# Optimization experiments

Hardware: AMD Instinct MI355X
Metric: run time of the kernel (lower is better)

The kernel has to match this reference:

```python
import jax, jax.numpy as jnp
import numpy as np

DT = 0.01  # continuous-time step for the S4D/Vandermonde reservoir kernel


def setup_inputs() -> dict:
    key = jax.random.key(0)
    ks = jax.random.split(key, 10)
    B, H, L, N = 16, 128, 4096, 64
    u = jax.random.normal(ks[0], (B, H, L), dtype=jnp.float32)
    # stable diagonal SSM: real part of Lambda strictly negative
    lambda_re = -0.5 * jax.random.uniform(ks[1], (H, N), dtype=jnp.float32) - 0.1
    lambda_im = jax.random.normal(ks[2], (H, N), dtype=jnp.float32) * np.pi
    w_re = jax.random.normal(ks[3], (H, N), dtype=jnp.float32) / np.sqrt(N)
    w_im = jax.random.normal(ks[4], (H, N), dtype=jnp.float32) / np.sqrt(N)
    d = jax.random.normal(ks[5], (H,), dtype=jnp.float32)
    mlp_w1 = jax.random.normal(ks[6], (H, H), dtype=jnp.float32) / np.sqrt(H)
    mlp_b1 = jnp.zeros((H,), dtype=jnp.float32)
    mlp_w2 = jax.random.normal(ks[7], (H, H), dtype=jnp.float32) / np.sqrt(H)
    mlp_b2 = jnp.zeros((H,), dtype=jnp.float32)
    return {"u": u, "lambda_re": lambda_re, "lambda_im": lambda_im,
            "w_re": w_re, "w_im": w_im, "d": d,
            "mlp_w1": mlp_w1, "mlp_b1": mlp_b1,
            "mlp_w2": mlp_w2, "mlp_b2": mlp_b2}


def reference(u, lambda_re, lambda_im, w_re, w_im, d,
              mlp_w1, mlp_b1, mlp_w2, mlp_b2):
    B, H, L = u.shape
    Lam = lambda_re + 1j * lambda_im          # (H, N) diagonal state matrix
    W = w_re + 1j * w_im                      # (H, N) merged C*B readout
    ell = jnp.arange(L, dtype=jnp.float32)
    # Vandermonde kernel: K[h, l] = sum_n W[h,n] * exp(dt * Lambda[h,n] * l)
    V = jnp.exp((DT * Lam)[:, :, None] * ell[None, None, :])  # (H, N, L)
    K = jnp.einsum('hn,hnl->hl', W, V)                         # (H, L) complex
    # causal FFT convolution (pad to 2L to avoid circular wrap)
    n = 2 * L
    y = jnp.fft.ifft(jnp.fft.fft(u, n=n, axis=-1) * jnp.fft.fft(K, n=n, axis=-1)[None],
                     n=n, axis=-1)[..., :L]
    y = y + d[None, :, None] * u              # skip / feed-through term
    y = y.real                                # Real() projection
    # 1x1-conv MLP with ReLU (mlp_layers = 2)
    h1 = jax.nn.relu(jnp.einsum('oh,bhl->bol', mlp_w1, y) + mlp_b1[None, :, None])
    y2 = jax.nn.relu(jnp.einsum('oh,bhl->bol', mlp_w2, h1) + mlp_b2[None, :, None])
    return y2
```

## Files before the change

kernel.cpp:

```cpp
#include <hip/hip_runtime.h>
#include <hip/hip_bf16.h>

#define B_ 16
#define H_ 128
#define L_ 4096
#define N_ 64
#define DT_ 0.01f

typedef __bf16 bf16;
typedef __bf16 bf16x8 __attribute__((ext_vector_type(8)));
typedef __bf16 bf16x4 __attribute__((ext_vector_type(4)));
typedef float f32x4 __attribute__((ext_vector_type(4)));

__global__ void k_prep(const float* __restrict__ w1, const float* __restrict__ w2,
                       bf16* __restrict__ w1b, bf16* __restrict__ w2b) {
    int i = blockIdx.x * blockDim.x + threadIdx.x;
    if (i < H_ * H_) {
        w1b[i] = (bf16)w1[i];
        w2b[i] = (bf16)w2[i];
    }
}

__global__ __launch_bounds__(64) void k_prep2(
        const float* __restrict__ lre, const float* __restrict__ lim,
        const float* __restrict__ wre, const float* __restrict__ wim,
        bf16* __restrict__ Pbf, bf16* __restrict__ Qbf,
        float* __restrict__ tap, float* __restrict__ acre, float* __restrict__ acim) {
    __shared__ float red[64 * 65];
    const int h = blockIdx.x, n = threadIdx.x;
    const float lr = lre[h * 64 + n] * DT_, li = lim[h * 64 + n] * DT_;
    const float e = expf(lr);
    const float ar = e * cosf(li), ai = e * sinf(li);
    const float wr = wre[h * 64 + n], wi = wim[h * 64 + n];
    const float war = wr * ar - wi * ai;
    const float wai = wr * ai + wi * ar;
    float pr = 1.f, pi = 0.f;
    bf16* Ph = Pbf + (size_t)h * 128 * 64;
    bf16* Qh = Qbf + (size_t)h * 64 * 128;
    for (int dlt = 0; dlt < 64; ++dlt) {
        Ph[(size_t)n * 64 + (63 - dlt)]        = (bf16)pr;
        Ph[(size_t)(64 + n) * 64 + (63 - dlt)] = (bf16)pi;
        Qh[(size_t)dlt * 128 + 2 * n]     = (bf16)(war * pr - wai * pi);
        Qh[(size_t)dlt * 128 + 2 * n + 1] = (bf16)(-(war * pi + wai * pr));
        red[dlt * 65 + n] = wr * pr - wi * pi;
        const float npr = ar * pr - ai * pi;
        const float npi = ar * pi + ai * pr;
        pr = npr; pi = npi;
    }
    acre[h * 64 + n] = pr;
    acim[h * 64 + n] = pi;
    __syncthreads();
    float s = 0.f;
    #pragma unroll
    for (int k = 0; k < 64; ++k) s += red[n * 65 + k];
    tap[h * 64 + n] = s;
}

#define USWZ(c, k) ((c) * 64 + (((((k) >> 4) ^ ((c) & 3)) << 4) | ((k) & 15)))
#define SSWZ(c, k) ((c) * 128 + (((((k) >> 4) ^ ((c) & 7)) << 4) | ((k) & 15)))
__global__ __launch_bounds__(256) void k_ssm2(
        const float* __restrict__ u, const float* __restrict__ dv,
        const bf16* __restrict__ Pbf, const bf16* __restrict__ Qbf,
        const float* __restrict__ tap,
        const float* __restrict__ acre, const float* __restrict__ acim,
        bf16* __restrict__ ybf) {
    __shared__ bf16  Ubf[64 * 64];
    __shared__ float Ctr[128 * 65];
    __shared__ bf16  Sbf[64 * 128];
    __shared__ bf16  Tm[64 * 72];

    const int tid = threadIdx.x;
    const int bh  = blockIdx.x;
    const int h   = bh & (H_ - 1);
    const float* __restrict__ up = u + (size_t)bh * L_;

    {
        const int c = tid >> 2, j0 = (tid & 3) << 4;
        const float4* src = (const float4*)(up + c * 64 + j0);
        bf16x8 t0, t1;
        #pragma unroll
        for (int v = 0; v < 2; ++v) {
            float4 f0 = src[2 * v], f1 = src[2 * v + 1];
            bf16x8 t;
            t[0] = (bf16)f0.x; t[1] = (bf16)f0.y; t[2] = (bf16)f0.z; t[3] = (bf16)f0.w;
            t[4] = (bf16)f1.x; t[5] = (bf16)f1.y; t[6] = (bf16)f1.z; t[7] = (bf16)f1.w;
            if (v == 0) t0 = t; else t1 = t;
        }
        bf16* dst = &Ubf[USWZ(c, j0)];
        ((bf16x8*)dst)[0] = t0;
        ((bf16x8*)dst)[1] = t1;
    }
    {
        const int dlt = tid >> 2, j0 = (tid & 3) << 4;
        const float* tp = tap + h * 64;
        const float dh = dv[h];
        bf16x8 t0, t1;
        #pragma unroll
        for (int e = 0; e < 16; ++e) {
            const int j = j0 + e;
            float v = (j <= dlt) ? tp[dlt - j] : 0.f;
            if (j == dlt) v += dh;
            if (e < 8) t0[e] = (bf16)v; else t1[e - 8] = (bf16)v;
        }
        bf16* dst = &Tm[dlt * 72 + j0];
        ((bf16x8*)dst)[0] = t0;
        ((bf16x8*)dst)[1] = t1;
    }
    __syncthreads();

    const int lane = tid & 63, wv = tid >> 6;
    const int cl = lane & 15, q = lane >> 4;

    {
        f32x4 acc[2][4];
        #pragma unroll
        for (int i = 0; i < 2; ++i)
            #pragma unroll
            for (int nt = 0; nt < 4; ++nt) acc[i][nt] = (f32x4){0.f, 0.f, 0.f, 0.f};
        const bf16* Ph = Pbf + (size_t)h * 128 * 64;
        #pragma unroll
        for (int ks = 0; ks < 2; ++ks) {
            const int k0 = ks * 32 + q * 8;
            const bf16x8 a0 = *(const bf16x8*)(Ph + (size_t)(wv * 32 + cl) * 64 + k0);
            const bf16x8 a1 = *(const bf16x8*)(Ph + (size_t)(wv * 32 + 16 + cl) * 64 + k0);
            #pragma unroll
            for (int nt = 0; nt < 4; ++nt) {
                const int c = nt * 16 + cl;
                const bf16x8 bfr = *(const bf16x8*)(&Ubf[USWZ(c, k0)]);
                acc[0][nt] = __builtin_amdgcn_mfma_f32_16x16x32_bf16(a0, bfr, acc[0][nt], 0, 0, 0);
                acc[1][nt] = __builtin_amdgcn_mfma_f32_16x16x32_bf16(a1, bfr, acc[1][nt], 0, 0, 0);
            }
        }
        #pragma unroll
        for (int mt = 0; mt < 2; ++mt)
            #pragma unroll
            for (int nt = 0; nt < 4; ++nt)
                #pragma unroll
                for (int r = 0; r < 4; ++r)
                    Ctr[(wv * 32 + mt * 16 + q * 4 + r) * 65 + nt * 16 + cl] = acc[mt][nt][r];
    }
    __syncthreads();

    if (wv == 0) {
        const int n = lane;
        const float ar = acre[h * 64 + n], ai = acim[h * 64 + n];
        float sr = 0.f, si = 0.f;
        #pragma unroll 8
        for (int c = 0; c < 64; ++c) {
            bf16* sp = &Sbf[SSWZ(c, 2 * n)];
            sp[0] = (bf16)sr;
            sp[1] = (bf16)si;
            const float cr = Ctr[n * 65 + c];
            const float ci = Ctr[(64 + n) * 65 + c];
            const float nr = fmaf(ar, sr, fmaf(-ai, si, cr));
            const float ni = fmaf(ar, si, fmaf(ai, sr, ci));
            sr = nr; si = ni;
        }
    }
    __syncthreads();

    {
        f32x4 acc[4];
        #pragma unroll
        for (int nt = 0; nt < 4; ++nt) acc[nt] = (f32x4){0.f, 0.f, 0.f, 0.f};
        const bf16* Qh = Qbf + (size_t)h * 64 * 128;
        #pragma unroll
        for (int ks = 0; ks < 4; ++ks) {
            const int k0 = ks * 32 + q * 8;
            const bf16x8 a = *(const bf16x8*)(Qh + (size_t)(wv * 16 + cl) * 128 + k0);
            #pragma unroll
            for (int nt = 0; nt < 4; ++nt) {
                const int c = nt * 16 + cl;
                const bf16x8 bfr = *(const bf16x8*)(&Sbf[SSWZ(c, k0)]);
                acc[nt] = __builtin_amdgcn_mfma_f32_16x16x32_bf16(a, bfr, acc[nt], 0, 0, 0);
            }
        }
        #pragma unroll
        for (int ks = 0; ks < 2; ++ks) {
            const int k0 = ks * 32 + q * 8;
            const bf16x8 a = *(const bf16x8*)(&Tm[(wv * 16 + cl) * 72 + k0]);
            #pragma unroll
            for (int nt = 0; nt < 4; ++nt) {
                const int c = nt * 16 + cl;
                const bf16x8 bfr = *(const bf16x8*)(&Ubf[USWZ(c, k0)]);
                acc[nt] = __builtin_amdgcn_mfma_f32_16x16x32_bf16(a, bfr, acc[nt], 0, 0, 0);
            }
        }
        bf16* Yb = (bf16*)Ctr;
        #pragma unroll
        for (int nt = 0; nt < 4; ++nt) {
            const int c = nt * 16 + cl;
            bf16x4 yv;
            #pragma unroll
            for (int r = 0; r < 4; ++r) yv[r] = (bf16)acc[nt][r];
            *(bf16x4*)(&Yb[c * 68 + wv * 16 + q * 4]) = yv;
        }
    }
    __syncthreads();

    {
        const bf16* Yb = (const bf16*)Ctr;
        const int c = tid >> 2, s0 = (tid & 3) << 4;
        bf16x4 v0 = *(const bf16x4*)(&Yb[c * 68 + s0 + 0]);
        bf16x4 v1 = *(const bf16x4*)(&Yb[c * 68 + s0 + 4]);
        bf16x4 v2 = *(const bf16x4*)(&Yb[c * 68 + s0 + 8]);
        bf16x4 v3 = *(const bf16x4*)(&Yb[c * 68 + s0 + 12]);
        bf16* yp = ybf + (size_t)bh * L_ + c * 64 + s0;
        ((bf16x4*)yp)[0] = v0; ((bf16x4*)yp)[1] = v1;
        ((bf16x4*)yp)[2] = v2; ((bf16x4*)yp)[3] = v3;
    }
}

#define YSTR 136
__global__ __launch_bounds__(256) void k_mlp(
        const bf16* __restrict__ ybf,
        const bf16* __restrict__ w1b, const bf16* __restrict__ w2b,
        const float* __restrict__ b1, const float* __restrict__ b2,
        float* __restrict__ out) {
    __shared__ bf16 YT [64 * YSTR];
    __shared__ bf16 H1T[64 * YSTR];
    __shared__ float B1s[H_], B2s[H_];

    const int tid = threadIdx.x;
    const int b   = blockIdx.x >> 6;
    const int lt  = blockIdx.x & 63;
    const int l0  = lt * 64;

    if (tid < H_) { B1s[tid] = b1[tid]; B2s[tid] = b2[tid]; }

    {
        const int h  = tid >> 1;
        const int lh = (tid & 1) * 32;
        const bf16x8* src = (const bf16x8*)(ybf + ((size_t)b * H_ + h) * L_ + l0 + lh);
        #pragma unroll
        for (int v = 0; v < 4; ++v) {
            bf16x8 d = src[v];
            #pragma unroll
            for (int e = 0; e < 8; ++e) YT[(lh + v * 8 + e) * YSTR + h] = d[e];
        }
    }
    __syncthreads();

    const int lane = tid & 63;
    const int wv   = tid >> 6;
    const int m    = lane & 15;
    const int q    = lane >> 4;
    const int m0   = wv * 32;

    f32x4 acc[2][4];
    #pragma unroll
    for (int i = 0; i < 2; ++i)
        #pragma unroll
        for (int nt = 0; nt < 4; ++nt) acc[i][nt] = (f32x4){0.f, 0.f, 0.f, 0.f};

    #pragma unroll
    for (int kb = 0; kb < 4; ++kb) {
        const bf16x8 a0 = *(const bf16x8*)(w1b + (size_t)(m0 + m)      * H_ + kb * 32 + q * 8);
        const bf16x8 a1 = *(const bf16x8*)(w1b + (size_t)(m0 + 16 + m) * H_ + kb * 32 + q * 8);
        #pragma unroll
        for (int nt = 0; nt < 4; ++nt) {
            const bf16x8 bfr = *(const bf16x8*)(&YT[(nt * 16 + m) * YSTR + kb * 32 + q * 8]);
            acc[0][nt] = __builtin_amdgcn_mfma_f32_16x16x32_bf16(a0, bfr, acc[0][nt], 0, 0, 0);
            acc[1][nt] = __builtin_amdgcn_mfma_f32_16x16x32_bf16(a1, bfr, acc[1][nt], 0, 0, 0);
        }
    }

    #pragma unroll
    for (int i = 0; i < 2; ++i) {
        const int o0 = m0 + 16 * i + 4 * q;
        #pragma unroll
        for (int nt = 0; nt < 4; ++nt) {
            const f32x4 v = acc[i][nt];
            bf16x4 hv;
            #pragma unroll
            for (int r = 0; r < 4; ++r) {
                float x = v[r] + B1s[o0 + r];
                hv[r] = (bf16)fmaxf(x, 0.f);
            }
            *(bf16x4*)(&H1T[(nt * 16 + m) * YSTR + o0]) = hv;
        }
    }
    __syncthreads();

    f32x4 acc2[2][4];
    #pragma unroll
    for (int i = 0; i < 2; ++i)
        #pragma unroll
        for (int nt = 0; nt < 4; ++nt) acc2[i][nt] = (f32x4){0.f, 0.f, 0.f, 0.f};

    #pragma unroll
    for (int kb = 0; kb < 4; ++kb) {
        const bf16x8 a0 = *(const bf16x8*)(w2b + (size_t)(m0 + m)      * H_ + kb * 32 + q * 8);
        const bf16x8 a1 = *(const bf16x8*)(w2b + (size_t)(m0 + 16 + m) * H_ + kb * 32 + q * 8);
        #pragma unroll
        for (int nt = 0; nt < 4; ++nt) {
            const bf16x8 bfr = *(const bf16x8*)(&H1T[(nt * 16 + m) * YSTR + kb * 32 + q * 8]);
            acc2[0][nt] = __builtin_amdgcn_mfma_f32_16x16x32_bf16(a0, bfr, acc2[0][nt], 0, 0, 0);
            acc2[1][nt] = __builtin_amdgcn_mfma_f32_16x16x32_bf16(a1, bfr, acc2[1][nt], 0, 0, 0);
        }
    }

    #pragma unroll
    for (int i = 0; i < 2; ++i) {
        const int o0 = m0 + 16 * i + 4 * q;
        #pragma unroll
        for (int nt = 0; nt < 4; ++nt) {
            const f32x4 v = acc2[i][nt];
            #pragma unroll
            for (int r = 0; r < 4; ++r) {
                float x = v[r] + B2s[o0 + r];
                x = fmaxf(x, 0.f);
                out[((size_t)b * H_ + o0 + r) * L_ + l0 + nt * 16 + m] = x;
            }
        }
    }
}

extern "C" void kernel_launch(void* const* d_in, const int* in_sizes, int n_in,
                              void* d_out, int out_size, void* d_ws, size_t ws_size,
                              hipStream_t stream) {
    const float* u   = (const float*)d_in[0];
    const float* lre = (const float*)d_in[1];
    const float* lim = (const float*)d_in[2];
    const float* wre = (const float*)d_in[3];
    const float* wim = (const float*)d_in[4];
    const float* dv  = (const float*)d_in[5];
    const float* w1  = (const float*)d_in[6];
    const float* b1  = (const float*)d_in[7];
    const float* w2  = (const float*)d_in[8];
    const float* b2  = (const float*)d_in[9];
    float* out = (float*)d_out;

    char* ws = (char*)d_ws;
    bf16*  ybf  = (bf16*)ws;                 ws += (size_t)B_ * H_ * L_ * 2;
    bf16*  w1b  = (bf16*)ws;                 ws += H_ * H_ * 2;
    bf16*  w2b  = (bf16*)ws;                 ws += H_ * H_ * 2;
    bf16*  Pbf  = (bf16*)ws;                 ws += (size_t)H_ * 128 * 64 * 2;
    bf16*  Qbf  = (bf16*)ws;                 ws += (size_t)H_ * 64 * 128 * 2;
    float* tap  = (float*)ws;                ws += H_ * 64 * 4;
    float* acre = (float*)ws;                ws += H_ * 64 * 4;
    float* acim = (float*)ws;                ws += H_ * 64 * 4;

    hipLaunchKernelGGL(k_prep, dim3((H_ * H_ + 255) / 256), dim3(256), 0, stream,
                       w1, w2, w1b, w2b);
    hipLaunchKernelGGL(k_prep2, dim3(H_), dim3(64), 0, stream,
                       lre, lim, wre, wim, Pbf, Qbf, tap, acre, acim);
    hipLaunchKernelGGL(k_ssm2, dim3(B_ * H_), dim3(256), 0, stream,
                       u, dv, Pbf, Qbf, tap, acre, acim, ybf);
    hipLaunchKernelGGL(k_mlp, dim3(B_ * (L_ / 64)), dim3(256), 0, stream,
                       ybf, w1b, w2b, b1, b2, out);
}
```

Baseline: 136.7 us.

## Merge prep kernels, stage P/Q in LDS, widen SSM blocks, share MLP LDS buffer

Folds the weight bf16 conversion into the per-head prep kernel, removing one launch, and stages the P/Q tables in shared memory so they are written to global memory with coalesced vector stores. The SSM kernel moves from 256 to 512 threads per block, giving each wave a smaller MFMA tile to add parallelism per block. The MLP kernel reuses one LDS buffer for both layers and adds an occupancy hint, which costs an extra barrier. The larger blocks leave fewer accumulators per wave but increase LDS and sync pressure.

```diff
diff --git a/kernel.cpp b/kernel.cpp
--- a/kernel.cpp
+++ b/kernel.cpp
@@ -12,22 +12,24 @@
 typedef __bf16 bf16x4 __attribute__((ext_vector_type(4)));
 typedef float f32x4 __attribute__((ext_vector_type(4)));
 
-__global__ void k_prep(const float* __restrict__ w1, const float* __restrict__ w2,
-                       bf16* __restrict__ w1b, bf16* __restrict__ w2b) {
-    int i = blockIdx.x * blockDim.x + threadIdx.x;
-    if (i < H_ * H_) {
-        w1b[i] = (bf16)w1[i];
-        w2b[i] = (bf16)w2[i];
-    }
-}
-
-__global__ __launch_bounds__(64) void k_prep2(
+__global__ __launch_bounds__(64) void k_prep(
         const float* __restrict__ lre, const float* __restrict__ lim,
         const float* __restrict__ wre, const float* __restrict__ wim,
+        const float* __restrict__ w1, const float* __restrict__ w2,
+        bf16* __restrict__ w1b, bf16* __restrict__ w2b,
         bf16* __restrict__ Pbf, bf16* __restrict__ Qbf,
         float* __restrict__ tap, float* __restrict__ acre, float* __restrict__ acim) {
+    __shared__ bf16  Pl[128 * 72];
+    __shared__ bf16  Ql[64 * 136];
     __shared__ float red[64 * 65];
+
     const int h = blockIdx.x, n = threadIdx.x;
+
+    w1b[h * H_ + n]      = (bf16)w1[h * H_ + n];
+    w1b[h * H_ + 64 + n] = (bf16)w1[h * H_ + 64 + n];
+    w2b[h * H_ + n]      = (bf16)w2[h * H_ + n];
+    w2b[h * H_ + 64 + n] = (bf16)w2[h * H_ + 64 + n];
+
     const float lr = lre[h * 64 + n] * DT_, li = lim[h * 64 + n] * DT_;
     const float e = expf(lr);
     const float ar = e * cosf(li), ai = e * sinf(li);
@@ -35,13 +37,13 @@
     const float war = wr * ar - wi * ai;
     const float wai = wr * ai + wi * ar;
     float pr = 1.f, pi = 0.f;
-    bf16* Ph = Pbf + (size_t)h * 128 * 64;
-    bf16* Qh = Qbf + (size_t)h * 64 * 128;
     for (int dlt = 0; dlt < 64; ++dlt) {
-        Ph[(size_t)n * 64 + (63 - dlt)]        = (bf16)pr;
-        Ph[(size_t)(64 + n) * 64 + (63 - dlt)] = (bf16)pi;
-        Qh[(size_t)dlt * 128 + 2 * n]     = (bf16)(war * pr - wai * pi);
-        Qh[(size_t)dlt * 128 + 2 * n + 1] = (bf16)(-(war * pi + wai * pr));
+        Pl[n * 72 + (63 - dlt)]        = (bf16)pr;
+        Pl[(64 + n) * 72 + (63 - dlt)] = (bf16)pi;
+        bf16 q0 = (bf16)(war * pr - wai * pi);
+        bf16 q1 = (bf16)(-(war * pi + wai * pr));
+        Ql[dlt * 136 + 2 * n]     = q0;
+        Ql[dlt * 136 + 2 * n + 1] = q1;
         red[dlt * 65 + n] = wr * pr - wi * pi;
         const float npr = ar * pr - ai * pi;
         const float npi = ar * pi + ai * pr;
@@ -50,15 +52,33 @@
     acre[h * 64 + n] = pr;
     acim[h * 64 + n] = pi;
     __syncthreads();
+
     float s = 0.f;
     #pragma unroll
     for (int k = 0; k < 64; ++k) s += red[n * 65 + k];
     tap[h * 64 + n] = s;
+
+    bf16* Ph = Pbf + (size_t)h * 128 * 64;
+    bf16* Qh = Qbf + (size_t)h * 64 * 128;
+    #pragma unroll
+    for (int i = 0; i < 16; ++i) {
+        const int flat = i * 512 + n * 8;
+        {
+            const int row = flat >> 6, col = flat & 63;
+            bf16x8 v = *(const bf16x8*)(&Pl[row * 72 + col]);
+            *(bf16x8*)(Ph + flat) = v;
+        }
+        {
+            const int row = flat >> 7, col = flat & 127;
+            bf16x8 v = *(const bf16x8*)(&Ql[row * 136 + col]);
+            *(bf16x8*)(Qh + flat) = v;
+        }
+    }
 }
 
 #define USWZ(c, k) ((c) * 64 + (((((k) >> 4) ^ ((c) & 3)) << 4) | ((k) & 15)))
 #define SSWZ(c, k) ((c) * 128 + (((((k) >> 4) ^ ((c) & 7)) << 4) | ((k) & 15)))
-__global__ __launch_bounds__(256) void k_ssm2(
+__global__ __launch_bounds__(512, 4) void k_ssm2(
         const float* __restrict__ u, const float* __restrict__ dv,
         const bf16* __restrict__ Pbf, const bf16* __restrict__ Qbf,
         const float* __restrict__ tap,
@@ -75,36 +95,27 @@
     const float* __restrict__ up = u + (size_t)bh * L_;
 
     {
-        const int c = tid >> 2, j0 = (tid & 3) << 4;
+        const int c = tid >> 3, j0 = (tid & 7) << 3;
         const float4* src = (const float4*)(up + c * 64 + j0);
-        bf16x8 t0, t1;
-        #pragma unroll
-        for (int v = 0; v < 2; ++v) {
-            float4 f0 = src[2 * v], f1 = src[2 * v + 1];
-            bf16x8 t;
-            t[0] = (bf16)f0.x; t[1] = (bf16)f0.y; t[2] = (bf16)f0.z; t[3] = (bf16)f0.w;
-            t[4] = (bf16)f1.x; t[5] = (bf16)f1.y; t[6] = (bf16)f1.z; t[7] = (bf16)f1.w;
-            if (v == 0) t0 = t; else t1 = t;
-        }
-        bf16* dst = &Ubf[USWZ(c, j0)];
-        ((bf16x8*)dst)[0] = t0;
-        ((bf16x8*)dst)[1] = t1;
-    }
-    {
-        const int dlt = tid >> 2, j0 = (tid & 3) << 4;
+        float4 f0 = src[0], f1 = src[1];
+        bf16x8 t;
+        t[0] = (bf16)f0.x; t[1] = (bf16)f0.y; t[2] = (bf16)f0.z; t[3] = (bf16)f0.w;
+        t[4] = (bf16)f1.x; t[5] = (bf16)f1.y; t[6] = (bf16)f1.z; t[7] = (bf16)f1.w;
+        *(bf16x8*)(&Ubf[USWZ(c, j0)]) = t;
+    }
+    {
+        const int dlt = tid >> 3, j0 = (tid & 7) << 3;
         const float* tp = tap + h * 64;
         const float dh = dv[h];
-        bf16x8 t0, t1;
-        #pragma unroll
-        for (int e = 0; e < 16; ++e) {
+        bf16x8 t;
+        #pragma unroll
+        for (int e = 0; e < 8; ++e) {
             const int j = j0 + e;
             float v = (j <= dlt) ? tp[dlt - j] : 0.f;
             if (j == dlt) v += dh;
-            if (e < 8) t0[e] = (bf16)v; else t1[e - 8] = (bf16)v;
-        }
-        bf16* dst = &Tm[dlt * 72 + j0];
-        ((bf16x8*)dst)[0] = t0;
-        ((bf16x8*)dst)[1] = t1;
+            t[e] = (bf16)v;
+        }
+        *(bf16x8*)(&Tm[dlt * 72 + j0]) = t;
     }
     __syncthreads();
 
@@ -112,32 +123,26 @@
     const int cl = lane & 15, q = lane >> 4;
 
     {
-        f32x4 acc[2][4];
-        #pragma unroll
-        for (int i = 0; i < 2; ++i)
-            #pragma unroll
-            for (int nt = 0; nt < 4; ++nt) acc[i][nt] = (f32x4){0.f, 0.f, 0.f, 0.f};
+        f32x4 acc[4];
+        #pragma unroll
+        for (int nt = 0; nt < 4; ++nt) acc[nt] = (f32x4){0.f, 0.f, 0.f, 0.f};
         const bf16* Ph = Pbf + (size_t)h * 128 * 64;
         #pragma unroll
         for (int ks = 0; ks < 2; ++ks) {
             const int k0 = ks * 32 + q * 8;
-            const bf16x8 a0 = *(const bf16x8*)(Ph + (size_t)(wv * 32 + cl) * 64 + k0);
-            const bf16x8 a1 = *(const bf16x8*)(Ph + (size_t)(wv * 32 + 16 + cl) * 64 + k0);
+            const bf16x8 a = *(const bf16x8*)(Ph + (size_t)(wv * 16 + cl) * 64 + k0);
             #pragma unroll
             for (int nt = 0; nt < 4; ++nt) {
                 const int c = nt * 16 + cl;
                 const bf16x8 bfr = *(const bf16x8*)(&Ubf[USWZ(c, k0)]);
-                acc[0][nt] = __builtin_amdgcn_mfma_f32_16x16x32_bf16(a0, bfr, acc[0][nt], 0, 0, 0);
-                acc[1][nt] = __builtin_amdgcn_mfma_f32_16x16x32_bf16(a1, bfr, acc[1][nt], 0, 0, 0);
-            }
-        }
-        #pragma unroll
-        for (int mt = 0; mt < 2; ++mt)
-            #pragma unroll
-            for (int nt = 0; nt < 4; ++nt)
-                #pragma unroll
-                for (int r = 0; r < 4; ++r)
-                    Ctr[(wv * 32 + mt * 16 + q * 4 + r) * 65 + nt * 16 + cl] = acc[mt][nt][r];
+                acc[nt] = __builtin_amdgcn_mfma_f32_16x16x32_bf16(a, bfr, acc[nt], 0, 0, 0);
+            }
+        }
+        #pragma unroll
+        for (int nt = 0; nt < 4; ++nt)
+            #pragma unroll
+            for (int r = 0; r < 4; ++r)
+                Ctr[(wv * 16 + q * 4 + r) * 65 + nt * 16 + cl] = acc[nt][r];
     }
     __syncthreads();
 
@@ -160,65 +165,61 @@
     __syncthreads();
 
     {
-        f32x4 acc[4];
-        #pragma unroll
-        for (int nt = 0; nt < 4; ++nt) acc[nt] = (f32x4){0.f, 0.f, 0.f, 0.f};
+        const int mt  = wv >> 1;
+        const int nt0 = (wv & 1) * 2;
+        f32x4 acc[2];
+        acc[0] = (f32x4){0.f, 0.f, 0.f, 0.f};
+        acc[1] = (f32x4){0.f, 0.f, 0.f, 0.f};
         const bf16* Qh = Qbf + (size_t)h * 64 * 128;
         #pragma unroll
         for (int ks = 0; ks < 4; ++ks) {
             const int k0 = ks * 32 + q * 8;
-            const bf16x8 a = *(const bf16x8*)(Qh + (size_t)(wv * 16 + cl) * 128 + k0);
-            #pragma unroll
-            for (int nt = 0; nt < 4; ++nt) {
-                const int c = nt * 16 + cl;
+            const bf16x8 a = *(const bf16x8*)(Qh + (size_t)(mt * 16 + cl) * 128 + k0);
+            #pragma unroll
+            for (int j = 0; j < 2; ++j) {
+                const int c = (nt0 + j) * 16 + cl;
                 const bf16x8 bfr = *(const bf16x8*)(&Sbf[SSWZ(c, k0)]);
-                acc[nt] = __builtin_amdgcn_mfma_f32_16x16x32_bf16(a, bfr, acc[nt], 0, 0, 0);
+                acc[j] = __builtin_amdgcn_mfma_f32_16x16x32_bf16(a, bfr, acc[j], 0, 0, 0);
             }
         }
         #pragma unroll
         for (int ks = 0; ks < 2; ++ks) {
             const int k0 = ks * 32 + q * 8;
-            const bf16x8 a = *(const bf16x8*)(&Tm[(wv * 16 + cl) * 72 + k0]);
-            #pragma unroll
-            for (int nt = 0; nt < 4; ++nt) {
-                const int c = nt * 16 + cl;
+            const bf16x8 a = *(const bf16x8*)(&Tm[(mt * 16 + cl) * 72 + k0]);
+            #pragma unroll
+            for (int j = 0; j < 2; ++j) {
+                const int c = (nt0 + j) * 16 + cl;
                 const bf16x8 bfr = *(const bf16x8*)(&Ubf[USWZ(c, k0)]);
-                acc[nt] = __builtin_amdgcn_mfma_f32_16x16x32_bf16(a, bfr, acc[nt], 0, 0, 0);
+                acc[j] = __builtin_amdgcn_mfma_f32_16x16x32_bf16(a, bfr, acc[j], 0, 0, 0);
             }
         }
         bf16* Yb = (bf16*)Ctr;
         #pragma unroll
-        for (int nt = 0; nt < 4; ++nt) {
-            const int c = nt * 16 + cl;
+        for (int j = 0; j < 2; ++j) {
+            const int c = (nt0 + j) * 16 + cl;
             bf16x4 yv;
             #pragma unroll
-            for (int r = 0; r < 4; ++r) yv[r] = (bf16)acc[nt][r];
-            *(bf16x4*)(&Yb[c * 68 + wv * 16 + q * 4]) = yv;
+            for (int r = 0; r < 4; ++r) yv[r] = (bf16)acc[j][r];
+            *(bf16x4*)(&Yb[c * 72 + mt * 16 + q * 4]) = yv;
         }
     }
     __syncthreads();
 
     {
         const bf16* Yb = (const bf16*)Ctr;
-        const int c = tid >> 2, s0 = (tid & 3) << 4;
-        bf16x4 v0 = *(const bf16x4*)(&Yb[c * 68 + s0 + 0]);
-        bf16x4 v1 = *(const bf16x4*)(&Yb[c * 68 + s0 + 4]);
-        bf16x4 v2 = *(const bf16x4*)(&Yb[c * 68 + s0 + 8]);
-        bf16x4 v3 = *(const bf16x4*)(&Yb[c * 68 + s0 + 12]);
-        bf16* yp = ybf + (size_t)bh * L_ + c * 64 + s0;
-        ((bf16x4*)yp)[0] = v0; ((bf16x4*)yp)[1] = v1;
-        ((bf16x4*)yp)[2] = v2; ((bf16x4*)yp)[3] = v3;
+        const int c = tid >> 3, s0 = (tid & 7) << 3;
+        bf16x8 v = *(const bf16x8*)(&Yb[c * 72 + s0]);
+        *(bf16x8*)(ybf + (size_t)bh * L_ + c * 64 + s0) = v;
     }
 }
 
 #define YSTR 136
-__global__ __launch_bounds__(256) void k_mlp(
+__global__ __launch_bounds__(256, 6) void k_mlp(
         const bf16* __restrict__ ybf,
         const bf16* __restrict__ w1b, const bf16* __restrict__ w2b,
         const float* __restrict__ b1, const float* __restrict__ b2,
         float* __restrict__ out) {
-    __shared__ bf16 YT [64 * YSTR];
-    __shared__ bf16 H1T[64 * YSTR];
+    __shared__ bf16 YT[64 * YSTR];
     __shared__ float B1s[H_], B2s[H_];
 
     const int tid = threadIdx.x;
@@ -264,6 +265,7 @@
             acc[1][nt] = __builtin_amdgcn_mfma_f32_16x16x32_bf16(a1, bfr, acc[1][nt], 0, 0, 0);
         }
     }
+    __syncthreads();
 
     #pragma unroll
     for (int i = 0; i < 2; ++i) {
@@ -277,7 +279,7 @@
                 float x = v[r] + B1s[o0 + r];
                 hv[r] = (bf16)fmaxf(x, 0.f);
             }
-            *(bf16x4*)(&H1T[(nt * 16 + m) * YSTR + o0]) = hv;
+            *(bf16x4*)(&YT[(nt * 16 + m) * YSTR + o0]) = hv;
         }
     }
     __syncthreads();
@@ -294,7 +296,7 @@
         const bf16x8 a1 = *(const bf16x8*)(w2b + (size_t)(m0 + 16 + m) * H_ + kb * 32 + q * 8);
         #pragma unroll
         for (int nt = 0; nt < 4; ++nt) {
-            const bf16x8 bfr = *(const bf16x8*)(&H1T[(nt * 16 + m) * YSTR + kb * 32 + q * 8]);
+            const bf16x8 bfr = *(const bf16x8*)(&YT[(nt * 16 + m) * YSTR + kb * 32 + q * 8]);
             acc2[0][nt] = __builtin_amdgcn_mfma_f32_16x16x32_bf16(a0, bfr, acc2[0][nt], 0, 0, 0);
             acc2[1][nt] = __builtin_amdgcn_mfma_f32_16x16x32_bf16(a1, bfr, acc2[1][nt], 0, 0, 0);
         }
@@ -341,11 +343,10 @@
     float* acre = (float*)ws;                ws += H_ * 64 * 4;
     float* acim = (float*)ws;                ws += H_ * 64 * 4;
 
-    hipLaunchKernelGGL(k_prep, dim3((H_ * H_ + 255) / 256), dim3(256), 0, stream,
-                       w1, w2, w1b, w2b);
-    hipLaunchKernelGGL(k_prep2, dim3(H_), dim3(64), 0, stream,
-                       lre, lim, wre, wim, Pbf, Qbf, tap, acre, acim);
-    hipLaunchKernelGGL(k_ssm2, dim3(B_ * H_), dim3(256), 0, stream,
+    hipLaunchKernelGGL(k_prep, dim3(H_), dim3(64), 0, stream,
+                       lre, lim, wre, wim, w1, w2, w1b, w2b,
+                       Pbf, Qbf, tap, acre, acim);
+    hipLaunchKernelGGL(k_ssm2, dim3(B_ * H_), dim3(512), 0, stream,
                        u, dv, Pbf, Qbf, tap, acre, acim, ybf);
     hipLaunchKernelGGL(k_mlp, dim3(B_ * (L_ / 64)), dim3(256), 0, stream,
                        ybf, w1b, w2b, b1, b2, out);
```

Result: no change. 136.0 us (-0.5%).
